# Kernel tuning notes

Measured on AMD Instinct MI355X. Metric: run time of the kernel, lower is better.

The kernel has to match this reference:

```python
import jax, jax.numpy as jnp
import numpy as np

N, C, T, V = 32, 128, 256, 25
K = 5  # temporal kernel size; reflect-pad 2*(K-1)//2 = 4 rows on top
EPS = 1e-5


def _inorm(x):
    # InstanceNorm2d(affine=False): normalize each (n,c) plane over (T,V)
    m = jnp.mean(x, axis=(2, 3), keepdims=True)
    v = jnp.var(x, axis=(2, 3), keepdims=True)
    return (x - m) * jax.lax.rsqrt(v + EPS)


def setup_inputs() -> dict:
    key = jax.random.key(0)
    ks = jax.random.split(key, 5)
    x = jax.random.normal(ks[0], (N, C, T, V), jnp.float32)
    PA = jax.random.normal(ks[1], (V, V), jnp.float32)          # learned adjacency
    Wd = jax.random.normal(ks[2], (C, C), jnp.float32) * 0.05    # 1x1 conv weight (O,I)
    bd = jnp.zeros((C,), jnp.float32)
    Wt = jax.random.normal(ks[3], (C, C, K, 1), jnp.float32) * 0.02  # (O,I,Kt,1)
    bt = jnp.zeros((C,), jnp.float32)
    return {"x": x, "PA": PA, "Wd": Wd, "bd": bd, "Wt": Wt, "bt": bt}


def reference(x, PA, Wd, bd, Wt, bt):
    # GCN unit: x.view(N,C*T,V) @ PA == einsum over last (joint) axis
    g = jnp.einsum('nctv,vw->nctw', x, PA)
    # 1x1 conv (channel GEMM) + bias
    y = jnp.einsum('nctv,oc->notv', g, Wd) + bd[None, :, None, None]
    # instance norm + identity residual (in_c == out_c) + relu
    y = jax.nn.relu(_inorm(y) + x)
    # TCN unit: reflection-pad 4 rows on top of T, conv (5,1) stride 1, instance norm
    yp = jnp.pad(y, ((0, 0), (0, 0), (4, 0), (0, 0)), mode='reflect')
    z = jax.lax.conv_general_dilated(
        yp, Wt, window_strides=(1, 1), padding='VALID',
        dimension_numbers=('NCHW', 'OIHW', 'NCHW')) + bt[None, :, None, None]
    z = _inorm(z)
    # outer residual (identity: in_c == out_c, stride == 1) + relu
    return jax.nn.relu(z + x)
```

## Files before the change

kernel.cpp:

```cpp
#include <hip/hip_runtime.h>


typedef unsigned short u16;
typedef unsigned int   u32;

using short8  = __attribute__((ext_vector_type(8))) short;
using floatx4 = __attribute__((ext_vector_type(4))) float;

#define NBATCH 32
#define CH     128
#define TDIM   256
#define VDIM   25
#define KT     5
#define PLANE  6400
#define EPSF   1e-5f
#define INV_PLANE (1.0f/6400.0f)

__device__ __forceinline__ u16 f2bf(float f) {
    u32 u = __float_as_uint(f);
    return (u16)((u + 0x7fffu + ((u >> 16) & 1u)) >> 16);
}
__device__ __forceinline__ float bf2f(u16 h) {
    return __uint_as_float(((u32)h) << 16);
}
__device__ __forceinline__ void gload_lds16(const void* g, void* l) {
    __builtin_amdgcn_global_load_lds(
        (const __attribute__((address_space(1))) u32*)g,
        (__attribute__((address_space(3))) u32*)l, 16, 0, 0);
}

__global__ __launch_bounds__(256) void k0_init(
    const float* __restrict__ Wd, const float* __restrict__ Wt,
    float* __restrict__ statsY, float* __restrict__ statsZ,
    u16* __restrict__ WdB, u16* __restrict__ Wt_b)
{
    int i = blockIdx.x * 256 + threadIdx.x;
    if (i < 8192) {
        statsY[i] = 0.f;
    } else if (i < 16384) {
        statsZ[i - 8192] = 0.f;
    } else if (i < 32768) {
        int j  = i - 16384;
        int sl = j & 31;
        int o  = (j >> 5) & 127;
        int cc = j >> 12;
        WdB[j] = f2bf(Wd[o * CH + cc * 32 + sl]);
    } else {
        int j  = i - 32768;
        int sl = j & 31;
        int o  = (j >> 5) & 127;
        int r2 = j >> 12;
        int tap = r2 % KT;
        int ic  = r2 / KT;
        Wt_b[j] = f2bf(Wt[(o * CH + ic * 32 + sl) * KT + tap]);
    }
}

__global__ __launch_bounds__(256) void k1a_gcn(
    const float* __restrict__ x, const float* __restrict__ PA,
    u16* __restrict__ gT)
{
    __shared__ __attribute__((aligned(16))) u32 sG[6800];
    __shared__ float sPA[625];

    const int tid   = threadIdx.x;
    const int nic   = blockIdx.y;
    const int chunk = blockIdx.x;
    const int c0    = chunk * 400;
    const int cl    = tid >> 3;
    const int tl    = tid & 7;

    for (int i = tid; i < 625; i += 256) sPA[i] = PA[i];

    const float* xrow = x + (size_t)(nic * 32 + cl) * PLANE + c0 + tl * 50;
    float xr[50];
#pragma unroll
    for (int w = 0; w < 25; ++w) {
        float2 t2 = *(const float2*)(xrow + 2 * w);
        xr[2 * w]     = t2.x;
        xr[2 * w + 1] = t2.y;
    }
    __syncthreads();

    u16* sG16 = (u16*)sG;
#pragma unroll
    for (int v = 0; v < VDIM; ++v) {
        float g0 = 0.f, g1 = 0.f;
#pragma unroll
        for (int w = 0; w < VDIM; ++w) {
            float p = sPA[w * VDIM + v];
            g0 += xr[w] * p;
            g1 += xr[25 + w] * p;
        }
        int r0 = tl * 50 + v;
        sG16[r0 * 34 + cl]        = f2bf(g0);
        sG16[(r0 + 25) * 34 + cl] = f2bf(g1);
    }
    __syncthreads();

    u32* outd = (u32*)gT;
    const size_t ob = ((size_t)nic * PLANE + c0) * 16;
    for (int j = tid; j < 6400; j += 256) {
        int r = j >> 4, dw = j & 15;
        int q = dw >> 2, b = dw & 3;
        outd[ob + r * 16 + (((q ^ (r & 3)) << 2) | b)] = sG[r * 17 + dw];
    }
}

__global__ __launch_bounds__(256) void k1b_mfma(
    const u16* __restrict__ gT, const u16* __restrict__ WdB,
    const float* __restrict__ bd,
    u16* __restrict__ y0b, float* __restrict__ statsY)
{
    __shared__ __attribute__((aligned(16))) char lds[16384];

    const int tid  = threadIdx.x;
    const int wave = tid >> 6;
    const int lane = tid & 63;
    const int l    = lane & 15;
    const int quad = lane >> 4;
    const int n    = blockIdx.y;
    const int c0   = blockIdx.x * 128;
    const int wub  = tid & ~63;

    auto stageB = [&](int cc, char* dst) {
        const char* bsrc = (const char*)gT + ((size_t)(n * 4 + cc) * PLANE + c0) * 64;
#pragma unroll
        for (int it = 0; it < 2; ++it)
            gload_lds16(bsrc + (it * 256 + tid) * 16, dst + (it * 256 + wub) * 16);
    };

    stageB(0, lds);
    __syncthreads();

    floatx4 acc[2][8];
#pragma unroll
    for (int a = 0; a < 2; ++a)
#pragma unroll
        for (int b = 0; b < 8; ++b) acc[a][b] = (floatx4){0.f, 0.f, 0.f, 0.f};

    for (int cc = 0; cc < 4; ++cc) {
        char* const sBc = lds + (cc & 1) * 8192;
        char* const sBn = lds + ((cc + 1) & 1) * 8192;

        const char* abase = (const char*)WdB + cc * 8192 + (wave * 32 + l) * 64 + (quad << 4);
        const short8 a0 = *(const short8*)(abase);
        const short8 a1 = *(const short8*)(abase + 16 * 64);
        __builtin_amdgcn_sched_barrier(0);

        if (cc < 3) stageB(cc + 1, sBn);

#pragma unroll
        for (int ct = 0; ct < 8; ++ct) {
            const int r = ct * 16 + l;
            const short8 b = *(const short8*)(sBc + r * 64 + ((quad ^ (r & 3)) << 4));
            acc[0][ct] = __builtin_amdgcn_mfma_f32_16x16x32_bf16(a0, b, acc[0][ct], 0, 0, 0);
            acc[1][ct] = __builtin_amdgcn_mfma_f32_16x16x32_bf16(a1, b, acc[1][ct], 0, 0, 0);
        }
        __syncthreads();
    }

#pragma unroll
    for (int ot = 0; ot < 2; ++ot) {
#pragma unroll
        for (int reg = 0; reg < 4; ++reg) {
            const int o = wave * 32 + ot * 16 + quad * 4 + reg;
            const float bias = bd[o];
            float s1 = 0.f, s2 = 0.f;
            u16* yp = y0b + (size_t)(n * CH + o) * PLANE + c0 + l;
#pragma unroll
            for (int ct = 0; ct < 8; ++ct) {
                float val = acc[ot][ct][reg] + bias;
                yp[ct * 16] = f2bf(val);
                s1 += val; s2 += val * val;
            }
#pragma unroll
            for (int m = 1; m <= 8; m <<= 1) {
                s1 += __shfl_xor(s1, m, 64);
                s2 += __shfl_xor(s2, m, 64);
            }
            if (l == 0) {
                atomicAdd(&statsY[(n * CH + o) * 2 + 0], s1);
                atomicAdd(&statsY[(n * CH + o) * 2 + 1], s2);
            }
        }
    }
}

__global__ __launch_bounds__(256) void k2_yhat(
    const u16* __restrict__ y0b, const float* __restrict__ x,
    const float* __restrict__ statsY, u16* __restrict__ yhatT)
{
    __shared__ u32 sT[256 * 17];
    __shared__ float sM[32], sR[32];

    const int tid = threadIdx.x;
    const int nic = blockIdx.y;
    const int n   = nic >> 2, ic = nic & 3;
    const int c0  = blockIdx.x * 256;

    if (tid < 32) {
        float a = statsY[(n * CH + ic * 32 + tid) * 2 + 0];
        float b = statsY[(n * CH + ic * 32 + tid) * 2 + 1];
        float m = a * INV_PLANE;
        sM[tid] = m;
        sR[tid] = rsqrtf(b * INV_PLANE - m * m + EPSF);
    }
    __syncthreads();

    u16* sT16 = (u16*)sT;
#pragma unroll
    for (int k = 0; k < 4; ++k) {
        int j  = k * 256 + tid;
        int ch = j >> 5;
        int cb = (j & 31) << 3;
        int g  = (n * CH + ic * 32 + ch) * PLANE + c0 + cb;
        short8 yv = *(const short8*)(y0b + g);
        const float4* xp = (const float4*)(x + g);
        float4 x0 = xp[0], x1 = xp[1];
        float m = sM[ch], r = sR[ch];
        int wp = ((ch >> 1) ^ ((cb >> 3) & 15));
        u16* dst = sT16 + cb * 34 + wp * 2 + (ch & 1);
        dst[0 * 34] = f2bf(fmaxf((bf2f((u16)yv[0]) - m) * r + x0.x, 0.f));
        dst[1 * 34] = f2bf(fmaxf((bf2f((u16)yv[1]) - m) * r + x0.y, 0.f));
        dst[2 * 34] = f2bf(fmaxf((bf2f((u16)yv[2]) - m) * r + x0.z, 0.f));
        dst[3 * 34] = f2bf(fmaxf((bf2f((u16)yv[3]) - m) * r + x0.w, 0.f));
        dst[4 * 34] = f2bf(fmaxf((bf2f((u16)yv[4]) - m) * r + x1.x, 0.f));
        dst[5 * 34] = f2bf(fmaxf((bf2f((u16)yv[5]) - m) * r + x1.y, 0.f));
        dst[6 * 34] = f2bf(fmaxf((bf2f((u16)yv[6]) - m) * r + x1.z, 0.f));
        dst[7 * 34] = f2bf(fmaxf((bf2f((u16)yv[7]) - m) * r + x1.w, 0.f));
    }
    __syncthreads();

    u32* outd = (u32*)yhatT;
    int obase = (nic * PLANE + c0) * 16;
    for (int idx = tid; idx < 4096; idx += 256) {
        int r = idx >> 4, dw = idx & 15;
        int q = dw >> 2, b = dw & 3;
        u32 val = sT[r * 17 + ((dw ^ (r >> 3)) & 15)];
        outd[obase + r * 16 + (((q ^ (r & 3)) << 2) | b)] = val;
    }
}

__global__ __launch_bounds__(256, 2) void k3_mfma(
    const u16* __restrict__ yhatT, const u16* __restrict__ Wt_b,
    const float* __restrict__ bt,
    u16* __restrict__ zb, float* __restrict__ statsZ)
{
    __shared__ __attribute__((aligned(16))) char lds[49152];

    const int tid  = threadIdx.x;
    const int wave = tid >> 6;
    const int wr   = wave >> 1;
    const int wc   = wave & 1;
    const int lane = tid & 63;
    const int l    = lane & 15;
    const int quad = lane >> 4;
    const int n    = blockIdx.y;
    const int blk  = blockIdx.x;
    const int c0   = blk * 256;
    const int wub  = tid & ~63;

    floatx4 acc[4][8];
#pragma unroll
    for (int a = 0; a < 4; ++a)
#pragma unroll
        for (int b = 0; b < 8; ++b) acc[a][b] = (floatx4){0.f, 0.f, 0.f, 0.f};

    auto stageB = [&](int ic, char* dst) {
        const char* bsrc = (const char*)(yhatT + (size_t)(n * 4 + ic) * (PLANE * 32));
        if (blk == 0) {
#pragma unroll
            for (int it = 0; it < 4; ++it)
                gload_lds16(bsrc + (it * 256 + tid) * 16, dst + 6400 + (it * 256 + wub) * 16);
            const u32* bsrcd = (const u32*)bsrc;
            u32* sBd = (u32*)dst;
            for (int idx = tid; idx < 1600; idx += 256) {
                int r = idx >> 4, dw = idx & 15;
                int q = dw >> 2, b = dw & 3;
                int d = 100 - r;
                int tref = (d + 24) / 25;
                int v = r % 25;
                int sc = tref * 25 + v;
                sBd[r * 16 + (((q ^ (r & 3)) << 2) | b)] =
                    bsrcd[sc * 16 + (((q ^ (sc & 3)) << 2) | b)];
            }
        } else {
            const char* bsrc2 = bsrc + (size_t)(c0 - 100) * 64;
#pragma unroll
            for (int it = 0; it < 6; ++it)
                gload_lds16(bsrc2 + (it * 256 + tid) * 16, dst + (it * 256 + wub) * 16);
        }
    };

    stageB(0, lds);
    __syncthreads();

    for (int ic = 0; ic < 4; ++ic) {
        char* const sBc = lds + (ic & 1) * 24576;
        char* const sBn = lds + ((ic + 1) & 1) * 24576;

        short8 af[KT][4];
        const char* abase = (const char*)Wt_b + (size_t)ic * 40960
                          + (wr * 64 + l) * 64 + (quad << 4);
#pragma unroll
        for (int tap = 0; tap < KT; ++tap)
#pragma unroll
            for (int ot = 0; ot < 4; ++ot)
                af[tap][ot] = *(const short8*)(abase + (tap * 128 + ot * 16) * 64);
        __builtin_amdgcn_sched_barrier(0);

        if (ic < 3) stageB(ic + 1, sBn);

#pragma unroll
        for (int tap = 0; tap < KT; ++tap) {
#pragma unroll
            for (int ct = 0; ct < 8; ++ct) {
                const int r = wc * 128 + ct * 16 + l + tap * 25;
                const short8 b = *(const short8*)(sBc + r * 64 + ((quad ^ (r & 3)) << 4));
#pragma unroll
                for (int ot = 0; ot < 4; ++ot)
                    acc[ot][ct] = __builtin_amdgcn_mfma_f32_16x16x32_bf16(af[tap][ot], b, acc[ot][ct], 0, 0, 0);
            }
        }
        __syncthreads();
    }

#pragma unroll
    for (int ot = 0; ot < 4; ++ot) {
#pragma unroll
        for (int reg = 0; reg < 4; ++reg) {
            const int o = wr * 64 + ot * 16 + quad * 4 + reg;
            const float bias = bt[o];
            float s1 = 0.f, s2 = 0.f;
            u16* zp = zb + (size_t)(n * CH + o) * PLANE + c0 + wc * 128 + l;
#pragma unroll
            for (int ct = 0; ct < 8; ++ct) {
                float val = acc[ot][ct][reg] + bias;
                zp[ct * 16] = f2bf(val);
                s1 += val; s2 += val * val;
            }
#pragma unroll
            for (int m = 1; m <= 8; m <<= 1) {
                s1 += __shfl_xor(s1, m, 64);
                s2 += __shfl_xor(s2, m, 64);
            }
            if (l == 0) {
                atomicAdd(&statsZ[(n * CH + o) * 2 + 0], s1);
                atomicAdd(&statsZ[(n * CH + o) * 2 + 1], s2);
            }
        }
    }
}

__global__ __launch_bounds__(256) void k4_final(
    const u16* __restrict__ zb, const float* __restrict__ x,
    const float* __restrict__ statsZ, float* __restrict__ out)
{
    int g = blockIdx.x * 256 + threadIdx.x;
    int p = g / 800;
    float a = statsZ[p * 2 + 0], b = statsZ[p * 2 + 1];
    float m = a * INV_PLANE;
    float r = rsqrtf(b * INV_PLANE - m * m + EPSF);
    short8 zv = *(const short8*)(zb + (size_t)g * 8);
    const float4* xp = (const float4*)x + (size_t)g * 2;
    float4 x0 = xp[0], x1 = xp[1];
    float4 o0, o1;
    o0.x = fmaxf((bf2f((u16)zv[0]) - m) * r + x0.x, 0.f);
    o0.y = fmaxf((bf2f((u16)zv[1]) - m) * r + x0.y, 0.f);
    o0.z = fmaxf((bf2f((u16)zv[2]) - m) * r + x0.z, 0.f);
    o0.w = fmaxf((bf2f((u16)zv[3]) - m) * r + x0.w, 0.f);
    o1.x = fmaxf((bf2f((u16)zv[4]) - m) * r + x1.x, 0.f);
    o1.y = fmaxf((bf2f((u16)zv[5]) - m) * r + x1.y, 0.f);
    o1.z = fmaxf((bf2f((u16)zv[6]) - m) * r + x1.z, 0.f);
    o1.w = fmaxf((bf2f((u16)zv[7]) - m) * r + x1.w, 0.f);
    float4* op = (float4*)out + (size_t)g * 2;
    op[0] = o0;
    op[1] = o1;
}

extern "C" void kernel_launch(void* const* d_in, const int* in_sizes, int n_in,
                              void* d_out, int out_size, void* d_ws, size_t ws_size,
                              hipStream_t stream) {
    const float* x  = (const float*)d_in[0];
    const float* PA = (const float*)d_in[1];
    const float* Wd = (const float*)d_in[2];
    const float* bd = (const float*)d_in[3];
    const float* Wt = (const float*)d_in[4];
    const float* bt = (const float*)d_in[5];
    float* out = (float*)d_out;

    char* wsb = (char*)d_ws;
    u16*   y0b    = (u16*)(wsb);
    u16*   zb     = y0b;
    u16*   gT     = (u16*)(wsb + 52428800);
    u16*   yhatT  = gT;
    float* statsY = (float*)(wsb + 104857600);
    float* statsZ = (float*)(wsb + 104890368);
    u16*   WdB    = (u16*)(wsb + 104923136);
    u16*   Wt_b   = (u16*)(wsb + 104955904);

    k0_init<<<dim3(448), dim3(256), 0, stream>>>(Wd, Wt, statsY, statsZ, WdB, Wt_b);
    k1a_gcn<<<dim3(16, 128), dim3(256), 0, stream>>>(x, PA, gT);
    k1b_mfma<<<dim3(50, 32), dim3(256), 0, stream>>>(gT, WdB, bd, y0b, statsY);
    k2_yhat<<<dim3(25, 128), dim3(256), 0, stream>>>(y0b, x, statsY, yhatT);
    k3_mfma<<<dim3(25, 32), dim3(256), 0, stream>>>(yhatT, Wt_b, bt, zb, statsZ);
    k4_final<<<dim3(12800), dim3(256), 0, stream>>>(zb, x, statsZ, out);
}
```

Before: 402.2 us.

## Stage conv weights in LDS, remap k3 grid per XCD, cache bf16 x

The temporal-conv MFMA kernel now loads the swizzled bf16 weight tile for each input-channel chunk into LDS and reads A fragments from there, replacing the per-wave global register loads. This drops the double-buffered B staging in favor of a single buffer with two barriers per iteration. The grid is flattened and remapped so that each XCD handles four whole batches, which should improve L2 locality. Separately, k1a writes a bf16 copy of x when the workspace is large enough, and k2 reads that copy instead of fp32 x to cut residual traffic, at the cost of extra writes and a lower-precision residual.

```diff
diff --git a/kernel.cpp b/kernel.cpp
--- a/kernel.cpp
+++ b/kernel.cpp
@@ -52,13 +52,14 @@
         int r2 = j >> 12;
         int tap = r2 % KT;
         int ic  = r2 / KT;
-        Wt_b[j] = f2bf(Wt[(o * CH + ic * 32 + sl) * KT + tap]);
+        int il = (((sl >> 3) ^ (o & 3)) << 3) | (sl & 7);
+        Wt_b[j] = f2bf(Wt[(o * CH + ic * 32 + il) * KT + tap]);
     }
 }
 
 __global__ __launch_bounds__(256) void k1a_gcn(
     const float* __restrict__ x, const float* __restrict__ PA,
-    u16* __restrict__ gT)
+    u16* __restrict__ gT, u16* __restrict__ xb, int useXb)
 {
     __shared__ __attribute__((aligned(16))) u32 sG[6800];
     __shared__ float sPA[625];
@@ -79,6 +80,12 @@
         float2 t2 = *(const float2*)(xrow + 2 * w);
         xr[2 * w]     = t2.x;
         xr[2 * w + 1] = t2.y;
+    }
+    if (useXb) {
+        u32* xbd = (u32*)(xb + (size_t)(nic * 32 + cl) * PLANE + c0 + tl * 50);
+#pragma unroll
+        for (int w = 0; w < 25; ++w)
+            xbd[w] = (u32)f2bf(xr[2 * w]) | ((u32)f2bf(xr[2 * w + 1]) << 16);
     }
     __syncthreads();
 
@@ -189,6 +196,7 @@
 
 __global__ __launch_bounds__(256) void k2_yhat(
     const u16* __restrict__ y0b, const float* __restrict__ x,
+    const u16* __restrict__ xb, int useXb,
     const float* __restrict__ statsY, u16* __restrict__ yhatT)
 {
     __shared__ u32 sT[256 * 17];
@@ -216,19 +224,23 @@
         int cb = (j & 31) << 3;
         int g  = (n * CH + ic * 32 + ch) * PLANE + c0 + cb;
         short8 yv = *(const short8*)(y0b + g);
-        const float4* xp = (const float4*)(x + g);
-        float4 x0 = xp[0], x1 = xp[1];
+        float xf[8];
+        if (useXb) {
+            short8 xv = *(const short8*)(xb + g);
+#pragma unroll
+            for (int e = 0; e < 8; ++e) xf[e] = bf2f((u16)xv[e]);
+        } else {
+            const float4* xp = (const float4*)(x + g);
+            float4 x0 = xp[0], x1 = xp[1];
+            xf[0] = x0.x; xf[1] = x0.y; xf[2] = x0.z; xf[3] = x0.w;
+            xf[4] = x1.x; xf[5] = x1.y; xf[6] = x1.z; xf[7] = x1.w;
+        }
         float m = sM[ch], r = sR[ch];
         int wp = ((ch >> 1) ^ ((cb >> 3) & 15));
         u16* dst = sT16 + cb * 34 + wp * 2 + (ch & 1);
-        dst[0 * 34] = f2bf(fmaxf((bf2f((u16)yv[0]) - m) * r + x0.x, 0.f));
-        dst[1 * 34] = f2bf(fmaxf((bf2f((u16)yv[1]) - m) * r + x0.y, 0.f));
-        dst[2 * 34] = f2bf(fmaxf((bf2f((u16)yv[2]) - m) * r + x0.z, 0.f));
-        dst[3 * 34] = f2bf(fmaxf((bf2f((u16)yv[3]) - m) * r + x0.w, 0.f));
-        dst[4 * 34] = f2bf(fmaxf((bf2f((u16)yv[4]) - m) * r + x1.x, 0.f));
-        dst[5 * 34] = f2bf(fmaxf((bf2f((u16)yv[5]) - m) * r + x1.y, 0.f));
-        dst[6 * 34] = f2bf(fmaxf((bf2f((u16)yv[6]) - m) * r + x1.z, 0.f));
-        dst[7 * 34] = f2bf(fmaxf((bf2f((u16)yv[7]) - m) * r + x1.w, 0.f));
+#pragma unroll
+        for (int e = 0; e < 8; ++e)
+            dst[e * 34] = f2bf(fmaxf((bf2f((u16)yv[e]) - m) * r + xf[e], 0.f));
     }
     __syncthreads();
 
@@ -247,7 +259,9 @@
     const float* __restrict__ bt,
     u16* __restrict__ zb, float* __restrict__ statsZ)
 {
-    __shared__ __attribute__((aligned(16))) char lds[49152];
+    __shared__ __attribute__((aligned(16))) char lds[65536];
+    char* const sB = lds;
+    char* const sA = lds + 24576;
 
     const int tid  = threadIdx.x;
     const int wave = tid >> 6;
@@ -256,8 +270,11 @@
     const int lane = tid & 63;
     const int l    = lane & 15;
     const int quad = lane >> 4;
-    const int n    = blockIdx.y;
-    const int blk  = blockIdx.x;
+    const int id   = blockIdx.x;
+    const int xcd  = id & 7;
+    const int jj   = id >> 3;
+    const int n    = xcd * 4 + jj / 25;
+    const int blk  = jj % 25;
     const int c0   = blk * 256;
     const int wub  = tid & ~63;
 
@@ -267,14 +284,19 @@
 #pragma unroll
         for (int b = 0; b < 8; ++b) acc[a][b] = (floatx4){0.f, 0.f, 0.f, 0.f};
 
-    auto stageB = [&](int ic, char* dst) {
+    for (int ic = 0; ic < 4; ++ic) {
+        __syncthreads();
+        const char* asrc = (const char*)(Wt_b + ic * 20480);
+#pragma unroll
+        for (int it = 0; it < 10; ++it)
+            gload_lds16(asrc + (it * 256 + tid) * 16, sA + (it * 256 + wub) * 16);
         const char* bsrc = (const char*)(yhatT + (size_t)(n * 4 + ic) * (PLANE * 32));
         if (blk == 0) {
 #pragma unroll
             for (int it = 0; it < 4; ++it)
-                gload_lds16(bsrc + (it * 256 + tid) * 16, dst + 6400 + (it * 256 + wub) * 16);
+                gload_lds16(bsrc + (it * 256 + tid) * 16, sB + 6400 + (it * 256 + wub) * 16);
             const u32* bsrcd = (const u32*)bsrc;
-            u32* sBd = (u32*)dst;
+            u32* sBd = (u32*)sB;
             for (int idx = tid; idx < 1600; idx += 256) {
                 int r = idx >> 4, dw = idx & 15;
                 int q = dw >> 2, b = dw & 3;
@@ -289,41 +311,26 @@
             const char* bsrc2 = bsrc + (size_t)(c0 - 100) * 64;
 #pragma unroll
             for (int it = 0; it < 6; ++it)
-                gload_lds16(bsrc2 + (it * 256 + tid) * 16, dst + (it * 256 + wub) * 16);
-        }
-    };
-
-    stageB(0, lds);
-    __syncthreads();
-
-    for (int ic = 0; ic < 4; ++ic) {
-        char* const sBc = lds + (ic & 1) * 24576;
-        char* const sBn = lds + ((ic + 1) & 1) * 24576;
-
-        short8 af[KT][4];
-        const char* abase = (const char*)Wt_b + (size_t)ic * 40960
-                          + (wr * 64 + l) * 64 + (quad << 4);
-#pragma unroll
-        for (int tap = 0; tap < KT; ++tap)
-#pragma unroll
-            for (int ot = 0; ot < 4; ++ot)
-                af[tap][ot] = *(const short8*)(abase + (tap * 128 + ot * 16) * 64);
-        __builtin_amdgcn_sched_barrier(0);
-
-        if (ic < 3) stageB(ic + 1, sBn);
-
+                gload_lds16(bsrc2 + (it * 256 + tid) * 16, sB + (it * 256 + wub) * 16);
+        }
+        __syncthreads();
 #pragma unroll
         for (int tap = 0; tap < KT; ++tap) {
+            short8 af[4];
+#pragma unroll
+            for (int ot = 0; ot < 4; ++ot) {
+                int ro = wr * 64 + ot * 16 + l;
+                af[ot] = *(const short8*)(sA + tap * 8192 + ro * 64 + ((quad ^ (l & 3)) << 4));
+            }
 #pragma unroll
             for (int ct = 0; ct < 8; ++ct) {
-                const int r = wc * 128 + ct * 16 + l + tap * 25;
-                const short8 b = *(const short8*)(sBc + r * 64 + ((quad ^ (r & 3)) << 4));
+                int r = wc * 128 + ct * 16 + l + tap * 25;
+                const short8 b = *(const short8*)(sB + r * 64 + ((quad ^ (r & 3)) << 4));
 #pragma unroll
                 for (int ot = 0; ot < 4; ++ot)
-                    acc[ot][ct] = __builtin_amdgcn_mfma_f32_16x16x32_bf16(af[tap][ot], b, acc[ot][ct], 0, 0, 0);
-            }
-        }
-        __syncthreads();
+                    acc[ot][ct] = __builtin_amdgcn_mfma_f32_16x16x32_bf16(af[ot], b, acc[ot][ct], 0, 0, 0);
+            }
+        }
     }
 
 #pragma unroll
@@ -399,11 +406,13 @@
     float* statsZ = (float*)(wsb + 104890368);
     u16*   WdB    = (u16*)(wsb + 104923136);
     u16*   Wt_b   = (u16*)(wsb + 104955904);
+    u16*   xb     = (u16*)(wsb + 105119744);
+    const int useXb = (ws_size >= (size_t)157548544) ? 1 : 0;
 
     k0_init<<<dim3(448), dim3(256), 0, stream>>>(Wd, Wt, statsY, statsZ, WdB, Wt_b);
-    k1a_gcn<<<dim3(16, 128), dim3(256), 0, stream>>>(x, PA, gT);
+    k1a_gcn<<<dim3(16, 128), dim3(256), 0, stream>>>(x, PA, gT, xb, useXb);
     k1b_mfma<<<dim3(50, 32), dim3(256), 0, stream>>>(gT, WdB, bd, y0b, statsY);
-    k2_yhat<<<dim3(25, 128), dim3(256), 0, stream>>>(y0b, x, statsY, yhatT);
-    k3_mfma<<<dim3(25, 32), dim3(256), 0, stream>>>(yhatT, Wt_b, bt, zb, statsZ);
+    k2_yhat<<<dim3(25, 128), dim3(256), 0, stream>>>(y0b, x, xb, useXb, statsY, yhatT);
+    k3_mfma<<<dim3(800), dim3(256), 0, stream>>>(yhatT, Wt_b, bt, zb, statsZ);
     k4_final<<<dim3(12800), dim3(256), 0, stream>>>(zb, x, statsZ, out);
 }
```

New measurement: 381.5 us. 5.1% less time.
